# Optimization experiments

Hardware: AMD Instinct MI355X
Metric: run time of the kernel (lower is better)

Reference implementation:

```python
import jax, jax.numpy as jnp
import numpy as np

N, E, D, L = 50000, 800000, 128, 2
EPS = 1e-7

def _logmap0(y):
    # Poincare ball (c=1) logmap at origin: artanh(||y||) * y / ||y||
    n = jnp.linalg.norm(y, axis=-1, keepdims=True)
    nc = jnp.clip(n, EPS, 1.0 - 1e-5)
    return jnp.arctanh(nc) * y / jnp.maximum(n, EPS)

def _expmap0(u):
    # Poincare ball (c=1) expmap at origin: tanh(||u||) * u / ||u||
    n = jnp.linalg.norm(u, axis=-1, keepdims=True)
    return jnp.tanh(n) * u / jnp.maximum(n, EPS)

def _l2norm(x):
    # F.normalize(p=2, dim=1)
    return x / jnp.maximum(jnp.linalg.norm(x, axis=1, keepdims=True), 1e-12)

def setup_inputs() -> dict:
    key = jax.random.key(0)
    ks = jax.random.split(key, 12)
    src = jax.random.randint(ks[0], (E,), 0, N)
    dst = jax.random.randint(ks[1], (E,), 0, N)
    e_emb = jax.random.normal(ks[2], (N, D), jnp.float32)
    b_emb = jax.random.normal(ks[3], (N, D), jnp.float32) * 0.1  # inside Poincare ball
    s_emb = jax.random.normal(ks[4], (N, D), jnp.float32)
    sc = 0.05
    eW = jax.random.normal(ks[5], (L, D, D), jnp.float32) * sc
    eB = jax.random.normal(ks[6], (L, D), jnp.float32) * sc
    bW = jax.random.normal(ks[7], (L, D, D), jnp.float32) * sc
    bB = jax.random.normal(ks[8], (L, D), jnp.float32) * sc
    sW = jax.random.normal(ks[9], (L, D, D), jnp.float32) * sc
    sB = jax.random.normal(ks[10], (L, D), jnp.float32) * sc
    return dict(e_emb=e_emb, b_emb=b_emb, s_emb=s_emb, eW=eW, eB=eB,
                bW=bW, bB=bB, sW=sW, sB=sB, src=src, dst=dst)

def reference(e_emb, b_emb, s_emb, eW, eB, bW, bB, sW, sB, src, dst):
    n_nodes = e_emb.shape[0]
    ones_e = jnp.ones(src.shape[0], jnp.float32)
    in_deg = jax.ops.segment_sum(ones_e, dst, num_segments=n_nodes)
    out_deg = jax.ops.segment_sum(ones_e, src, num_segments=n_nodes)
    # DGL GraphConv norm='both': D_out^{-1/2} (sum over in-neighbors) D_in^{-1/2}
    norm_out = jnp.where(out_deg > 0, out_deg ** -0.5, 0.0)[:, None]
    norm_in = jnp.where(in_deg > 0, in_deg ** -0.5, 0.0)[:, None]
    inv_in = jnp.where(in_deg > 0, 1.0 / in_deg, 0.0)[:, None]  # mean reduce

    def agg_sum(h):
        return jax.ops.segment_sum(h[src], dst, num_segments=n_nodes)

    for l in range(L):
        # Euclidean branch: GraphConv(norm='both') then LeakyReLU(0.2)
        h = agg_sum(e_emb * norm_out) * norm_in
        e_emb = jax.nn.leaky_relu(h @ eW[l].T + eB[l], negative_slope=0.2)
        # Hyperbolic branch: logmap0 -> Linear -> neighbor mean -> expmap0
        tan_b = _logmap0(b_emb) @ bW[l].T + bB[l]
        b_emb = _expmap0(agg_sum(tan_b) * inv_in)
        # Spherical branch: normalize -> Linear -> neighbor mean -> normalize
        tan_s = _l2norm(s_emb) @ sW[l].T + sB[l]
        s_emb = _l2norm(agg_sum(tan_s) * inv_in)
    return (e_emb, b_emb, s_emb)
```

## Files before the change

kernel.cpp:

```cpp
#include <hip/hip_runtime.h>
#include <math.h>

#define DD 128
#define PSTRIDE 384

typedef _Float16 half8 __attribute__((ext_vector_type(8)));
typedef float floatx4 __attribute__((ext_vector_type(4)));

__device__ __forceinline__ float g16_sum(float x) {
#pragma unroll
  for (int m = 8; m >= 1; m >>= 1) x += __shfl_xor(x, m, 64);
  return x;
}
__device__ __forceinline__ int wave_sum_i(int x) {
#pragma unroll
  for (int m = 32; m >= 1; m >>= 1) x += __shfl_xor(x, m, 64);
  return x;
}

__device__ __forceinline__ void gemm0_tile(int part, int rb, const float* __restrict__ A,
                                           const float* __restrict__ Wf, const float* __restrict__ Bb,
                                           const float* __restrict__ norm_out,
                                           _Float16* __restrict__ Q, int N) {
  int t = threadIdx.x, lane = t & 63, w = t >> 6;
  int m = lane & 15, quad = lane >> 4, c0 = w * 32;
  int rbase = rb * 64;
  _Float16* Qo = Q + part * DD;
  half8 bf[2][4];
#pragma unroll
  for (int tj = 0; tj < 2; ++tj)
#pragma unroll
    for (int kk = 0; kk < 4; ++kk) {
      const float* wp = &Wf[(c0 + tj * 16 + m) * DD + kk * 32 + quad * 8];
      float4 w0 = *(const float4*)wp;
      float4 w1 = *(const float4*)(wp + 4);
      half8 hv;
      hv[0] = (_Float16)w0.x; hv[1] = (_Float16)w0.y; hv[2] = (_Float16)w0.z; hv[3] = (_Float16)w0.w;
      hv[4] = (_Float16)w1.x; hv[5] = (_Float16)w1.y; hv[6] = (_Float16)w1.z; hv[7] = (_Float16)w1.w;
      bf[tj][kk] = hv;
    }
  float bias0 = 0.f, bias1 = 0.f;
  if (part) { bias0 = Bb[c0 + m]; bias1 = Bb[c0 + 16 + m]; }
#pragma unroll
  for (int r = 0; r < 4; ++r) {
    int row0 = r * 16;
    int arow = rbase + row0 + m; if (arow >= N) arow = N - 1;
    const float* Ap = A + (size_t)arow * DD;
    half8 af[4];
    float nsq = 0.f;
#pragma unroll
    for (int kk = 0; kk < 4; ++kk) {
      float4 x0 = *(const float4*)&Ap[kk * 32 + quad * 8];
      float4 x1 = *(const float4*)&Ap[kk * 32 + quad * 8 + 4];
      if (part)
        nsq += x0.x * x0.x + x0.y * x0.y + x0.z * x0.z + x0.w * x0.w +
               x1.x * x1.x + x1.y * x1.y + x1.z * x1.z + x1.w * x1.w;
      half8 a;
      a[0] = (_Float16)x0.x; a[1] = (_Float16)x0.y; a[2] = (_Float16)x0.z; a[3] = (_Float16)x0.w;
      a[4] = (_Float16)x1.x; a[5] = (_Float16)x1.y; a[6] = (_Float16)x1.z; a[7] = (_Float16)x1.w;
      af[kk] = a;
    }
    float fr = 1.f;
    if (part) {
      nsq += __shfl_xor(nsq, 16, 64);
      nsq += __shfl_xor(nsq, 32, 64);
      float n = sqrtf(nsq);
      if (part == 1) {
        float nc = fminf(fmaxf(n, 1e-7f), 1.0f - 1e-5f);
        fr = atanhf(nc) / fmaxf(n, 1e-7f);
      } else {
        fr = 1.0f / fmaxf(n, 1e-12f);
      }
    }
    floatx4 acc0 = {0.f, 0.f, 0.f, 0.f}, acc1 = {0.f, 0.f, 0.f, 0.f};
#pragma unroll
    for (int kk = 0; kk < 4; ++kk) {
      acc0 = __builtin_amdgcn_mfma_f32_16x16x32_f16(af[kk], bf[0][kk], acc0, 0, 0, 0);
      acc1 = __builtin_amdgcn_mfma_f32_16x16x32_f16(af[kk], bf[1][kk], acc1, 0, 0, 0);
    }
    int vrow = rbase + row0 + quad * 4;
#pragma unroll
    for (int reg = 0; reg < 4; ++reg) {
      int v = vrow + reg;
      float fshfl = __shfl(fr, quad * 4 + reg, 64);
      if (v < N) {
        float sc = part ? fshfl : norm_out[v];
        Qo[(size_t)v * PSTRIDE + c0 + m]      = (_Float16)(acc0[reg] * sc + bias0);
        Qo[(size_t)v * PSTRIDE + c0 + 16 + m] = (_Float16)(acc1[reg] * sc + bias1);
      }
    }
  }
}

__device__ __forceinline__ void gemm_tile(int part, int rb, const _Float16* __restrict__ P,
                                          const float* __restrict__ Wf, const float* __restrict__ Bb,
                                          const float* __restrict__ norm_out,
                                          _Float16* __restrict__ Q, int N) {
  int t = threadIdx.x, lane = t & 63, w = t >> 6;
  int m = lane & 15, quad = lane >> 4, c0 = w * 32;
  int rbase = rb * 64;
  const _Float16* Ain = P + part * DD;
  _Float16* Qo = Q + part * DD;
  half8 bf[2][4];
#pragma unroll
  for (int tj = 0; tj < 2; ++tj)
#pragma unroll
    for (int kk = 0; kk < 4; ++kk) {
      const float* wp = &Wf[(c0 + tj * 16 + m) * DD + kk * 32 + quad * 8];
      float4 w0 = *(const float4*)wp;
      float4 w1 = *(const float4*)(wp + 4);
      half8 hv;
      hv[0] = (_Float16)w0.x; hv[1] = (_Float16)w0.y; hv[2] = (_Float16)w0.z; hv[3] = (_Float16)w0.w;
      hv[4] = (_Float16)w1.x; hv[5] = (_Float16)w1.y; hv[6] = (_Float16)w1.z; hv[7] = (_Float16)w1.w;
      bf[tj][kk] = hv;
    }
  float bias0 = 0.f, bias1 = 0.f;
  if (part) { bias0 = Bb[c0 + m]; bias1 = Bb[c0 + 16 + m]; }
#pragma unroll
  for (int r = 0; r < 4; ++r) {
    int row0 = r * 16;
    int arow = rbase + row0 + m; if (arow >= N) arow = N - 1;
    const _Float16* Ap = Ain + (size_t)arow * PSTRIDE;
    floatx4 acc0 = {0.f, 0.f, 0.f, 0.f}, acc1 = {0.f, 0.f, 0.f, 0.f};
#pragma unroll
    for (int kk = 0; kk < 4; ++kk) {
      half8 af = *(const half8*)&Ap[kk * 32 + quad * 8];
      acc0 = __builtin_amdgcn_mfma_f32_16x16x32_f16(af, bf[0][kk], acc0, 0, 0, 0);
      acc1 = __builtin_amdgcn_mfma_f32_16x16x32_f16(af, bf[1][kk], acc1, 0, 0, 0);
    }
    int vrow = rbase + row0 + quad * 4;
#pragma unroll
    for (int reg = 0; reg < 4; ++reg) {
      int v = vrow + reg;
      if (v < N) {
        float sc = part ? 1.f : norm_out[v];
        Qo[(size_t)v * PSTRIDE + c0 + m]      = (_Float16)(acc0[reg] * sc + bias0);
        Qo[(size_t)v * PSTRIDE + c0 + 16 + m] = (_Float16)(acc1[reg] * sc + bias1);
      }
    }
  }
}

__global__ __launch_bounds__(256) void deg_gemmbs_kernel(
    const int* __restrict__ src, const int* __restrict__ dst,
    int* __restrict__ out8, int* __restrict__ in8, int* __restrict__ rank8, int E, int N,
    const float* __restrict__ b0, const float* __restrict__ s0,
    const float* __restrict__ bW, const float* __restrict__ sW,
    const float* __restrict__ bB, const float* __restrict__ sB,
    float* __restrict__ norm_out_unused, _Float16* __restrict__ Q, int DB, int GBt) {
  int bx = blockIdx.x;
  if (bx < DB) {
    int g = bx * 256 + (int)threadIdx.x;
    int e0i = g * 4;
    if (e0i + 3 < E) {
      int4 s4 = ((const int4*)src)[g];
      int4 d4 = ((const int4*)dst)[g];
      atomicAdd(&out8[((e0i    ) & 7) * N + s4.x], 1);
      atomicAdd(&out8[((e0i + 1) & 7) * N + s4.y], 1);
      atomicAdd(&out8[((e0i + 2) & 7) * N + s4.z], 1);
      atomicAdd(&out8[((e0i + 3) & 7) * N + s4.w], 1);
      int4 r;
      r.x = atomicAdd(&in8[((e0i    ) & 7) * N + d4.x], 1);
      r.y = atomicAdd(&in8[((e0i + 1) & 7) * N + d4.y], 1);
      r.z = atomicAdd(&in8[((e0i + 2) & 7) * N + d4.z], 1);
      r.w = atomicAdd(&in8[((e0i + 3) & 7) * N + d4.w], 1);
      ((int4*)rank8)[g] = r;
    } else if (e0i < E) {
      for (int e = e0i; e < E; ++e) {
        atomicAdd(&out8[(e & 7) * N + src[e]], 1);
        rank8[e] = atomicAdd(&in8[(e & 7) * N + dst[e]], 1);
      }
    }
  } else {
    int gt = bx - DB;
    int part = 1 + gt / GBt, rb = gt % GBt;
    const float* A  = (part == 1) ? b0 : s0;
    const float* Wf = (part == 1) ? bW : sW;
    const float* Bb = (part == 1) ? bB : sB;
    gemm0_tile(part, rb, A, Wf, Bb, norm_out_unused, Q, N);
  }
}

__global__ void norms_psum_kernel(const int* __restrict__ in8, const int* __restrict__ out8,
                                  int* __restrict__ in_deg, float* __restrict__ norm_in,
                                  float* __restrict__ norm_out, float* __restrict__ inv_in,
                                  int* __restrict__ part, int N) {
  __shared__ int wsum[4];
  int t = threadIdx.x, lane = t & 63, w = t >> 6;
  int i = blockIdx.x * 256 + t;
  int di = 0;
  if (i < N) {
    int dq = 0;
#pragma unroll
    for (int h = 0; h < 8; ++h) { di += in8[h * N + i]; dq += out8[h * N + i]; }
    in_deg[i] = di;
    norm_in[i]  = di > 0 ? 1.0f / sqrtf((float)di) : 0.0f;
    norm_out[i] = dq > 0 ? 1.0f / sqrtf((float)dq) : 0.0f;
    inv_in[i]   = di > 0 ? 1.0f / (float)di : 0.0f;
  }
  int s = wave_sum_i(di);
  if (lane == 0) wsum[w] = s;
  __syncthreads();
  if (t == 0) part[blockIdx.x] = wsum[0] + wsum[1] + wsum[2] + wsum[3];
}

__global__ void part_scan_kernel(int* __restrict__ part, int nb) {
  __shared__ int wsum[4];
  int t = threadIdx.x, lane = t & 63, w = t >> 6;
  int x = (t < nb) ? part[t] : 0;
  int v = x;
#pragma unroll
  for (int off = 1; off < 64; off <<= 1) {
    int y = __shfl_up(v, off, 64);
    if (lane >= off) v += y;
  }
  if (lane == 63) wsum[w] = v;
  __syncthreads();
  int base = 0;
  for (int j = 0; j < w; ++j) base += wsum[j];
  if (t < nb) part[t] = base + v - x;
}

__global__ void local_scan_kernel(const int* __restrict__ deg, const int* __restrict__ part,
                                  int* __restrict__ row_off, int* __restrict__ in8,
                                  int N, int E) {
  __shared__ int wsum[4];
  int t = threadIdx.x, lane = t & 63, w = t >> 6;
  int i = blockIdx.x * 256 + t;
  int x = (i < N) ? deg[i] : 0;
  int v = x;
#pragma unroll
  for (int off = 1; off < 64; off <<= 1) {
    int y = __shfl_up(v, off, 64);
    if (lane >= off) v += y;
  }
  if (lane == 63) wsum[w] = v;
  __syncthreads();
  int base = 0;
  for (int j = 0; j < w; ++j) base += wsum[j];
  if (i < N) {
    int ro = part[blockIdx.x] + base + v - x;
    row_off[i] = ro;
    int cum = ro;
#pragma unroll
    for (int h = 0; h < 8; ++h) {
      int cb = in8[h * N + i];
      in8[h * N + i] = cum;
      cum += cb;
    }
  }
  if (blockIdx.x == 0 && t == 0) row_off[N] = E;
}

__global__ __launch_bounds__(256) void fill_gemme_kernel(
    const int* __restrict__ src, const int* __restrict__ dst,
    const int* __restrict__ rank8, const int* __restrict__ bin_base,
    int* __restrict__ csr, int E,
    const float* __restrict__ e0, const float* __restrict__ eW,
    const float* __restrict__ norm_out, _Float16* __restrict__ Q, int N, int FB, int GBt) {
  int bx = blockIdx.x;
  if (bx < FB) {
    int g = bx * 256 + (int)threadIdx.x;
    int e0i = g * 4;
    if (e0i + 3 < E) {
      int4 s4 = ((const int4*)src)[g];
      int4 d4 = ((const int4*)dst)[g];
      int4 r4 = ((const int4*)rank8)[g];
      csr[bin_base[((e0i    ) & 7) * N + d4.x] + r4.x] = s4.x;
      csr[bin_base[((e0i + 1) & 7) * N + d4.y] + r4.y] = s4.y;
      csr[bin_base[((e0i + 2) & 7) * N + d4.z] + r4.z] = s4.z;
      csr[bin_base[((e0i + 3) & 7) * N + d4.w] + r4.w] = s4.w;
    } else if (e0i < E) {
      for (int e = e0i; e < E; ++e)
        csr[bin_base[(e & 7) * N + dst[e]] + rank8[e]] = src[e];
    }
  } else {
    gemm0_tile(0, bx - FB, e0, eW, nullptr, norm_out, Q, N);
  }
}

__global__ __launch_bounds__(256) void gemm3_kernel(const _Float16* __restrict__ P,
                                                    const float* __restrict__ eWl,
                                                    const float* __restrict__ bWl,
                                                    const float* __restrict__ sWl,
                                                    const float* __restrict__ bBl,
                                                    const float* __restrict__ sBl,
                                                    const float* __restrict__ norm_out,
                                                    _Float16* __restrict__ Q, int N, int GBt) {
  int gt = blockIdx.x;
  int part = gt / GBt, rb = gt % GBt;
  const float* Wf = (part == 0) ? eWl : (part == 1 ? bWl : sWl);
  const float* Bb = (part == 1) ? bBl : sBl;
  gemm_tile(part, rb, P, Wf, Bb, norm_out, Q, N);
}

__global__ __launch_bounds__(256) void agg_fused_kernel(
    const _Float16* __restrict__ Q, const int* __restrict__ row_off,
    const int* __restrict__ csr, const float* __restrict__ norm_in,
    const float* __restrict__ inv_in, const float* __restrict__ eBias,
    float* __restrict__ oe, float* __restrict__ ob, float* __restrict__ os,
    _Float16* __restrict__ Pnext, int N, int write_pack, int write_out) {
  int lane = threadIdx.x & 63;
  int v = blockIdx.x * 4 + (threadIdx.x >> 6);
  if (v >= N) return;
  int g = lane >> 4, q = lane & 15;
  int beg = row_off[v], end = row_off[v + 1];
  float eacc[8], bacc[8], sacc[8];
#pragma unroll
  for (int j = 0; j < 8; ++j) { eacc[j] = 0.f; bacc[j] = 0.f; sacc[j] = 0.f; }
  int i = beg;
  for (; i + 8 <= end; i += 8) {
    int na = csr[i + g], nb2 = csr[i + 4 + g];
    const _Float16* ra = Q + (size_t)na * PSTRIDE + q * 8;
    const _Float16* rb = Q + (size_t)nb2 * PSTRIDE + q * 8;
    half8 ea = *(const half8*)ra;
    half8 e2 = *(const half8*)rb;
    half8 ba = *(const half8*)(ra + 128);
    half8 b2 = *(const half8*)(rb + 128);
    half8 sa = *(const half8*)(ra + 256);
    half8 s2 = *(const half8*)(rb + 256);
#pragma unroll
    for (int j = 0; j < 8; ++j) {
      eacc[j] += (float)ea[j]; eacc[j] += (float)e2[j];
      bacc[j] += (float)ba[j]; bacc[j] += (float)b2[j];
      sacc[j] += (float)sa[j]; sacc[j] += (float)s2[j];
    }
  }
  if (i + 4 <= end) {
    int na = csr[i + g];
    const _Float16* rp = Q + (size_t)na * PSTRIDE + q * 8;
    half8 ev = *(const half8*)rp;
    half8 bv = *(const half8*)(rp + 128);
    half8 sv = *(const half8*)(rp + 256);
#pragma unroll
    for (int j = 0; j < 8; ++j) {
      eacc[j] += (float)ev[j];
      bacc[j] += (float)bv[j];
      sacc[j] += (float)sv[j];
    }
    i += 4;
  }
  if (i + g < end) {
    int na = csr[i + g];
    const _Float16* rp = Q + (size_t)na * PSTRIDE + q * 8;
    half8 ev = *(const half8*)rp;
    half8 bv = *(const half8*)(rp + 128);
    half8 sv = *(const half8*)(rp + 256);
#pragma unroll
    for (int j = 0; j < 8; ++j) {
      eacc[j] += (float)ev[j];
      bacc[j] += (float)bv[j];
      sacc[j] += (float)sv[j];
    }
  }
#pragma unroll
  for (int j = 0; j < 8; ++j) {
    eacc[j] += __shfl_xor(eacc[j], 16, 64);
    eacc[j] += __shfl_xor(eacc[j], 32, 64);
    bacc[j] += __shfl_xor(bacc[j], 16, 64);
    bacc[j] += __shfl_xor(bacc[j], 32, 64);
    sacc[j] += __shfl_xor(sacc[j], 16, 64);
    sacc[j] += __shfl_xor(sacc[j], 32, 64);
  }
  float ni = norm_in[v], iv = inv_in[v];
  const float4* ebp = (const float4*)eBias;
  float4 eb0 = ebp[q * 2], eb1 = ebp[q * 2 + 1];
  float bias[8] = {eb0.x, eb0.y, eb0.z, eb0.w, eb1.x, eb1.y, eb1.z, eb1.w};
  float h[8], ub[8], us[8];
  float ss2 = 0.f;
#pragma unroll
  for (int j = 0; j < 8; ++j) {
    float tt = eacc[j] * ni + bias[j];
    h[j] = tt > 0.f ? tt : 0.2f * tt;
    ub[j] = bacc[j] * iv;
    us[j] = sacc[j] * iv; ss2 += us[j] * us[j];
  }
  float ns = sqrtf(g16_sum(ss2));
  float fs = 1.0f / fmaxf(ns, 1e-12f);
  if (write_out) {
    float bs2 = 0.f;
#pragma unroll
    for (int j = 0; j < 8; ++j) bs2 += ub[j] * ub[j];
    float nb = sqrtf(g16_sum(bs2));
    float fb = tanhf(nb) / fmaxf(nb, 1e-7f);
    if (g == 0) {
      float4* p = (float4*)(oe + (size_t)v * DD);
      p[q * 2]     = make_float4(h[0], h[1], h[2], h[3]);
      p[q * 2 + 1] = make_float4(h[4], h[5], h[6], h[7]);
    } else if (g == 1) {
      float4* p = (float4*)(ob + (size_t)v * DD);
      p[q * 2]     = make_float4(ub[0] * fb, ub[1] * fb, ub[2] * fb, ub[3] * fb);
      p[q * 2 + 1] = make_float4(ub[4] * fb, ub[5] * fb, ub[6] * fb, ub[7] * fb);
    } else if (g == 2) {
      float4* p = (float4*)(os + (size_t)v * DD);
      p[q * 2]     = make_float4(us[0] * fs, us[1] * fs, us[2] * fs, us[3] * fs);
      p[q * 2 + 1] = make_float4(us[4] * fs, us[5] * fs, us[6] * fs, us[7] * fs);
    }
  }
  if (write_pack && g == 3) {
    half8 he, hb, hs;
#pragma unroll
    for (int j = 0; j < 8; ++j) {
      he[j] = (_Float16)h[j];
      hb[j] = (_Float16)ub[j];
      hs[j] = (_Float16)(us[j] * fs);
    }
    _Float16* Pr = Pnext + (size_t)v * PSTRIDE + q * 8;
    *(half8*)&Pr[0]   = he;
    *(half8*)&Pr[128] = hb;
    *(half8*)&Pr[256] = hs;
  }
}

extern "C" void kernel_launch(void* const* d_in, const int* in_sizes, int n_in,
                              void* d_out, int out_size, void* d_ws, size_t ws_size,
                              hipStream_t stream) {
  const float* e0 = (const float*)d_in[0];
  const float* b0 = (const float*)d_in[1];
  const float* s0 = (const float*)d_in[2];
  const float* eW = (const float*)d_in[3];
  const float* eB = (const float*)d_in[4];
  const float* bW = (const float*)d_in[5];
  const float* bB = (const float*)d_in[6];
  const float* sW = (const float*)d_in[7];
  const float* sB = (const float*)d_in[8];
  const int* src = (const int*)d_in[9];
  const int* dst = (const int*)d_in[10];
  int N = in_sizes[0] / DD;
  int E = in_sizes[9];
  int L = in_sizes[3] / (DD * DD);

  char* w = (char*)d_ws;
  int* in_deg8  = (int*)w; w += (size_t)8 * N * 4;
  int* out_deg8 = (int*)w; w += (size_t)8 * N * 4;
  int* rank8    = (int*)w; w += (size_t)E * 4;
  int* in_deg   = (int*)w; w += (size_t)N * 4;
  int* row_off  = (int*)w; w += (size_t)(N + 4) * 4;
  int* pscan    = (int*)w; w += (size_t)1024 * 4;
  int* csr      = (int*)w; w += (size_t)E * 4;
  float* norm_in  = (float*)w; w += (size_t)N * 4;
  float* norm_out = (float*)w; w += (size_t)N * 4;
  float* inv_in   = (float*)w; w += (size_t)N * 4;
  w = (char*)(((size_t)w + 255) & ~(size_t)255);
  _Float16* P = (_Float16*)w; w += (size_t)N * PSTRIDE * 2;
  _Float16* Q = (_Float16*)w; w += (size_t)N * PSTRIDE * 2;

  float* oe = (float*)d_out;
  float* ob = oe + (size_t)N * DD;
  float* os = ob + (size_t)N * DD;

  int DB  = (E + 1023) / 1024;
  int ABt = (N + 3) / 4;
  int GBt = (N + 63) / 64;
  int NC  = (N + 255) / 256;

  hipMemsetAsync(d_ws, 0, (size_t)16 * N * 4, stream);
  deg_gemmbs_kernel<<<DB + 2 * GBt, 256, 0, stream>>>(src, dst, out_deg8, in_deg8, rank8, E, N,
                                                      b0, s0, bW, sW, bB, sB, norm_out, Q, DB, GBt);
  norms_psum_kernel<<<NC, 256, 0, stream>>>(in_deg8, out_deg8, in_deg,
                                            norm_in, norm_out, inv_in, pscan, N);
  part_scan_kernel<<<1, 256, 0, stream>>>(pscan, NC);
  local_scan_kernel<<<NC, 256, 0, stream>>>(in_deg, pscan, row_off, in_deg8, N, E);
  fill_gemme_kernel<<<DB + GBt, 256, 0, stream>>>(src, dst, rank8, in_deg8, csr, E,
                                                  e0, eW, norm_out, Q, N, DB, GBt);
  agg_fused_kernel<<<ABt, 256, 0, stream>>>(Q, row_off, csr, norm_in, inv_in, eB,
                                            oe, ob, os, P, N,
                                            (L > 1) ? 1 : 0, (L == 1) ? 1 : 0);
  for (int l = 1; l < L; ++l) {
    size_t lo = (size_t)l * DD * DD;
    gemm3_kernel<<<3 * GBt, 256, 0, stream>>>(P, eW + lo, bW + lo, sW + lo,
                                              bB + (size_t)l * DD, sB + (size_t)l * DD,
                                              norm_out, Q, N, GBt);
    agg_fused_kernel<<<ABt, 256, 0, stream>>>(Q, row_off, csr, norm_in, inv_in,
                                              eB + (size_t)l * DD, oe, ob, os, P, N,
                                              (l < L - 1) ? 1 : 0, (l == L - 1) ? 1 : 0);
  }
}
```

Measured before the change: 522.1 us.

## Move b/s layer-0 GEMMs from degree kernel into CSR fill kernel, scalarize edges

The hyperbolic and spherical layer-0 GEMM tiles no longer run in the degree-counting kernel. They now run alongside the Euclidean GEMM in the CSR fill kernel, which launches all three GEMM parts together. The degree and fill edge loops change from four vectorized edges per thread to one edge per thread. This undoes the earlier overlap of the b/s GEMMs with the atomic-heavy degree pass, gives the degree kernel a simpler launch, and makes the fill kernel larger.

```diff
diff --git a/kernel.cpp b/kernel.cpp
--- a/kernel.cpp
+++ b/kernel.cpp
@@ -16,6 +16,88 @@
 #pragma unroll
   for (int m = 32; m >= 1; m >>= 1) x += __shfl_xor(x, m, 64);
   return x;
+}
+
+__global__ void deg_kernel(const int* __restrict__ src, const int* __restrict__ dst,
+                           int* __restrict__ out8, int* __restrict__ in8,
+                           int* __restrict__ rank8, int E, int N) {
+  int e = blockIdx.x * 256 + threadIdx.x;
+  if (e < E) {
+    int h = e & 7;
+    atomicAdd(&out8[h * N + src[e]], 1);
+    rank8[e] = atomicAdd(&in8[h * N + dst[e]], 1);
+  }
+}
+
+__global__ void norms_psum_kernel(const int* __restrict__ in8, const int* __restrict__ out8,
+                                  int* __restrict__ in_deg, float* __restrict__ norm_in,
+                                  float* __restrict__ norm_out, float* __restrict__ inv_in,
+                                  int* __restrict__ part, int N) {
+  __shared__ int wsum[4];
+  int t = threadIdx.x, lane = t & 63, w = t >> 6;
+  int i = blockIdx.x * 256 + t;
+  int di = 0;
+  if (i < N) {
+    int dq = 0;
+#pragma unroll
+    for (int h = 0; h < 8; ++h) { di += in8[h * N + i]; dq += out8[h * N + i]; }
+    in_deg[i] = di;
+    norm_in[i]  = di > 0 ? 1.0f / sqrtf((float)di) : 0.0f;
+    norm_out[i] = dq > 0 ? 1.0f / sqrtf((float)dq) : 0.0f;
+    inv_in[i]   = di > 0 ? 1.0f / (float)di : 0.0f;
+  }
+  int s = wave_sum_i(di);
+  if (lane == 0) wsum[w] = s;
+  __syncthreads();
+  if (t == 0) part[blockIdx.x] = wsum[0] + wsum[1] + wsum[2] + wsum[3];
+}
+
+__global__ void part_scan_kernel(int* __restrict__ part, int nb) {
+  __shared__ int wsum[4];
+  int t = threadIdx.x, lane = t & 63, w = t >> 6;
+  int x = (t < nb) ? part[t] : 0;
+  int v = x;
+#pragma unroll
+  for (int off = 1; off < 64; off <<= 1) {
+    int y = __shfl_up(v, off, 64);
+    if (lane >= off) v += y;
+  }
+  if (lane == 63) wsum[w] = v;
+  __syncthreads();
+  int base = 0;
+  for (int j = 0; j < w; ++j) base += wsum[j];
+  if (t < nb) part[t] = base + v - x;
+}
+
+__global__ void local_scan_kernel(const int* __restrict__ deg, const int* __restrict__ part,
+                                  int* __restrict__ row_off, int* __restrict__ in8,
+                                  int N, int E) {
+  __shared__ int wsum[4];
+  int t = threadIdx.x, lane = t & 63, w = t >> 6;
+  int i = blockIdx.x * 256 + t;
+  int x = (i < N) ? deg[i] : 0;
+  int v = x;
+#pragma unroll
+  for (int off = 1; off < 64; off <<= 1) {
+    int y = __shfl_up(v, off, 64);
+    if (lane >= off) v += y;
+  }
+  if (lane == 63) wsum[w] = v;
+  __syncthreads();
+  int base = 0;
+  for (int j = 0; j < w; ++j) base += wsum[j];
+  if (i < N) {
+    int ro = part[blockIdx.x] + base + v - x;
+    row_off[i] = ro;
+    int cum = ro;
+#pragma unroll
+    for (int h = 0; h < 8; ++h) {
+      int cb = in8[h * N + i];
+      in8[h * N + i] = cum;
+      cum += cb;
+    }
+  }
+  if (blockIdx.x == 0 && t == 0) row_off[N] = E;
 }
 
 __device__ __forceinline__ void gemm0_tile(int part, int rb, const float* __restrict__ A,
@@ -141,141 +223,28 @@
   }
 }
 
-__global__ __launch_bounds__(256) void deg_gemmbs_kernel(
-    const int* __restrict__ src, const int* __restrict__ dst,
-    int* __restrict__ out8, int* __restrict__ in8, int* __restrict__ rank8, int E, int N,
-    const float* __restrict__ b0, const float* __restrict__ s0,
-    const float* __restrict__ bW, const float* __restrict__ sW,
-    const float* __restrict__ bB, const float* __restrict__ sB,
-    float* __restrict__ norm_out_unused, _Float16* __restrict__ Q, int DB, int GBt) {
-  int bx = blockIdx.x;
-  if (bx < DB) {
-    int g = bx * 256 + (int)threadIdx.x;
-    int e0i = g * 4;
-    if (e0i + 3 < E) {
-      int4 s4 = ((const int4*)src)[g];
-      int4 d4 = ((const int4*)dst)[g];
-      atomicAdd(&out8[((e0i    ) & 7) * N + s4.x], 1);
-      atomicAdd(&out8[((e0i + 1) & 7) * N + s4.y], 1);
-      atomicAdd(&out8[((e0i + 2) & 7) * N + s4.z], 1);
-      atomicAdd(&out8[((e0i + 3) & 7) * N + s4.w], 1);
-      int4 r;
-      r.x = atomicAdd(&in8[((e0i    ) & 7) * N + d4.x], 1);
-      r.y = atomicAdd(&in8[((e0i + 1) & 7) * N + d4.y], 1);
-      r.z = atomicAdd(&in8[((e0i + 2) & 7) * N + d4.z], 1);
-      r.w = atomicAdd(&in8[((e0i + 3) & 7) * N + d4.w], 1);
-      ((int4*)rank8)[g] = r;
-    } else if (e0i < E) {
-      for (int e = e0i; e < E; ++e) {
-        atomicAdd(&out8[(e & 7) * N + src[e]], 1);
-        rank8[e] = atomicAdd(&in8[(e & 7) * N + dst[e]], 1);
-      }
-    }
-  } else {
-    int gt = bx - DB;
-    int part = 1 + gt / GBt, rb = gt % GBt;
-    const float* A  = (part == 1) ? b0 : s0;
-    const float* Wf = (part == 1) ? bW : sW;
-    const float* Bb = (part == 1) ? bB : sB;
-    gemm0_tile(part, rb, A, Wf, Bb, norm_out_unused, Q, N);
-  }
-}
-
-__global__ void norms_psum_kernel(const int* __restrict__ in8, const int* __restrict__ out8,
-                                  int* __restrict__ in_deg, float* __restrict__ norm_in,
-                                  float* __restrict__ norm_out, float* __restrict__ inv_in,
-                                  int* __restrict__ part, int N) {
-  __shared__ int wsum[4];
-  int t = threadIdx.x, lane = t & 63, w = t >> 6;
-  int i = blockIdx.x * 256 + t;
-  int di = 0;
-  if (i < N) {
-    int dq = 0;
-#pragma unroll
-    for (int h = 0; h < 8; ++h) { di += in8[h * N + i]; dq += out8[h * N + i]; }
-    in_deg[i] = di;
-    norm_in[i]  = di > 0 ? 1.0f / sqrtf((float)di) : 0.0f;
-    norm_out[i] = dq > 0 ? 1.0f / sqrtf((float)dq) : 0.0f;
-    inv_in[i]   = di > 0 ? 1.0f / (float)di : 0.0f;
-  }
-  int s = wave_sum_i(di);
-  if (lane == 0) wsum[w] = s;
-  __syncthreads();
-  if (t == 0) part[blockIdx.x] = wsum[0] + wsum[1] + wsum[2] + wsum[3];
-}
-
-__global__ void part_scan_kernel(int* __restrict__ part, int nb) {
-  __shared__ int wsum[4];
-  int t = threadIdx.x, lane = t & 63, w = t >> 6;
-  int x = (t < nb) ? part[t] : 0;
-  int v = x;
-#pragma unroll
-  for (int off = 1; off < 64; off <<= 1) {
-    int y = __shfl_up(v, off, 64);
-    if (lane >= off) v += y;
-  }
-  if (lane == 63) wsum[w] = v;
-  __syncthreads();
-  int base = 0;
-  for (int j = 0; j < w; ++j) base += wsum[j];
-  if (t < nb) part[t] = base + v - x;
-}
-
-__global__ void local_scan_kernel(const int* __restrict__ deg, const int* __restrict__ part,
-                                  int* __restrict__ row_off, int* __restrict__ in8,
-                                  int N, int E) {
-  __shared__ int wsum[4];
-  int t = threadIdx.x, lane = t & 63, w = t >> 6;
-  int i = blockIdx.x * 256 + t;
-  int x = (i < N) ? deg[i] : 0;
-  int v = x;
-#pragma unroll
-  for (int off = 1; off < 64; off <<= 1) {
-    int y = __shfl_up(v, off, 64);
-    if (lane >= off) v += y;
-  }
-  if (lane == 63) wsum[w] = v;
-  __syncthreads();
-  int base = 0;
-  for (int j = 0; j < w; ++j) base += wsum[j];
-  if (i < N) {
-    int ro = part[blockIdx.x] + base + v - x;
-    row_off[i] = ro;
-    int cum = ro;
-#pragma unroll
-    for (int h = 0; h < 8; ++h) {
-      int cb = in8[h * N + i];
-      in8[h * N + i] = cum;
-      cum += cb;
-    }
-  }
-  if (blockIdx.x == 0 && t == 0) row_off[N] = E;
-}
-
-__global__ __launch_bounds__(256) void fill_gemme_kernel(
+__global__ __launch_bounds__(256) void fill_gemm0_kernel(
     const int* __restrict__ src, const int* __restrict__ dst,
     const int* __restrict__ rank8, const int* __restrict__ bin_base,
     int* __restrict__ csr, int E,
-    const float* __restrict__ e0, const float* __restrict__ eW,
+    const float* __restrict__ e0, const float* __restrict__ b0, const float* __restrict__ s0,
+    const float* __restrict__ eW, const float* __restrict__ bW, const float* __restrict__ sW,
+    const float* __restrict__ bB, const float* __restrict__ sB,
     const float* __restrict__ norm_out, _Float16* __restrict__ Q, int N, int FB, int GBt) {
   int bx = blockIdx.x;
   if (bx < FB) {
-    int g = bx * 256 + (int)threadIdx.x;
-    int e0i = g * 4;
-    if (e0i + 3 < E) {
-      int4 s4 = ((const int4*)src)[g];
-      int4 d4 = ((const int4*)dst)[g];
-      int4 r4 = ((const int4*)rank8)[g];
-      csr[bin_base[((e0i    ) & 7) * N + d4.x] + r4.x] = s4.x;
-      csr[bin_base[((e0i + 1) & 7) * N + d4.y] + r4.y] = s4.y;
-      csr[bin_base[((e0i + 2) & 7) * N + d4.z] + r4.z] = s4.z;
-      csr[bin_base[((e0i + 3) & 7) * N + d4.w] + r4.w] = s4.w;
-    } else if (e0i < E) {
-      for (int e = e0i; e < E; ++e)
-        csr[bin_base[(e & 7) * N + dst[e]] + rank8[e]] = src[e];
+    int e = bx * 256 + (int)threadIdx.x;
+    if (e < E) {
+      int d = dst[e];
+      csr[bin_base[(e & 7) * N + d] + rank8[e]] = src[e];
     }
   } else {
-    gemm0_tile(0, bx - FB, e0, eW, nullptr, norm_out, Q, N);
+    int gt = bx - FB;
+    int part = gt / GBt, rb = gt % GBt;
+    const float* A  = (part == 0) ? e0 : (part == 1 ? b0 : s0);
+    const float* Wf = (part == 0) ? eW : (part == 1 ? bW : sW);
+    const float* Bb = (part == 1) ? bB : sB;
+    gemm0_tile(part, rb, A, Wf, Bb, norm_out, Q, N);
   }
 }
 
@@ -449,20 +418,20 @@
   float* ob = oe + (size_t)N * DD;
   float* os = ob + (size_t)N * DD;
 
-  int DB  = (E + 1023) / 1024;
+  int EB  = (E + 255) / 256;
   int ABt = (N + 3) / 4;
   int GBt = (N + 63) / 64;
   int NC  = (N + 255) / 256;
 
   hipMemsetAsync(d_ws, 0, (size_t)16 * N * 4, stream);
-  deg_gemmbs_kernel<<<DB + 2 * GBt, 256, 0, stream>>>(src, dst, out_deg8, in_deg8, rank8, E, N,
-                                                      b0, s0, bW, sW, bB, sB, norm_out, Q, DB, GBt);
+  deg_kernel<<<EB, 256, 0, stream>>>(src, dst, out_deg8, in_deg8, rank8, E, N);
   norms_psum_kernel<<<NC, 256, 0, stream>>>(in_deg8, out_deg8, in_deg,
                                             norm_in, norm_out, inv_in, pscan, N);
   part_scan_kernel<<<1, 256, 0, stream>>>(pscan, NC);
   local_scan_kernel<<<NC, 256, 0, stream>>>(in_deg, pscan, row_off, in_deg8, N, E);
-  fill_gemme_kernel<<<DB + GBt, 256, 0, stream>>>(src, dst, rank8, in_deg8, csr, E,
-                                                  e0, eW, norm_out, Q, N, DB, GBt);
+  fill_gemm0_kernel<<<EB + 3 * GBt, 256, 0, stream>>>(src, dst, rank8, in_deg8, csr, E,
+                                                      e0, b0, s0, eW, bW, sW, bB, sB,
+                                                      norm_out, Q, N, EB, GBt);
   agg_fused_kernel<<<ABt, 256, 0, stream>>>(Q, row_off, csr, norm_in, inv_in, eB,
                                             oe, ob, os, P, N,
                                             (L > 1) ? 1 : 0, (L == 1) ? 1 : 0);
```

Result: no change. 523.7 us (+0.3%).
